# Performance work log

Hardware: AMD Instinct MI355X
Metric: run time of the kernel (lower is better)

Reference implementation:

```python
import jax, jax.numpy as jnp
import numpy as np
from jax import lax

N_QUBITS = 8
DIM = 256  # 2**8 amplitudes
NUM_BLOCKS = 16
DEPTH = 1
ALPHA = 0.5
BATCH = 512

# Z-sign tables: qubit 0 is the most-significant bit of the flattened state index
_bits = (np.arange(DIM)[:, None] >> (N_QUBITS - 1 - np.arange(N_QUBITS))) & 1  # (256, 8)
_SIGNS = jnp.asarray(1.0 - 2.0 * _bits, dtype=jnp.float32)  # (256, 8)
_pairs = [(i, j) for i in range(N_QUBITS) for j in range(i + 1, N_QUBITS)]
_PAIR_SIGNS = jnp.stack([_SIGNS[:, i] * _SIGNS[:, j] for (i, j) in _pairs], axis=1)  # (256, 28)


def _apply_ry(state, c, s, q):
    # state: (N, 256) real (RY and CNOT keep the state real); gate on qubit q
    dl, dr = 2 ** q, 2 ** (N_QUBITS - 1 - q)
    st = state.reshape(-1, dl, 2, dr)
    s0, s1 = st[:, :, 0, :], st[:, :, 1, :]
    c_, s_ = c[:, None, None], s[:, None, None]
    n0 = c_ * s0 - s_ * s1
    n1 = s_ * s0 + c_ * s1
    return jnp.stack([n0, n1], axis=2).reshape(-1, DIM)


def _apply_cnot_chain(state, i):
    # CNOT control=i, target=i+1 (adjacent qubits)
    dl, dr = 2 ** i, 2 ** (N_QUBITS - 2 - i)
    st = state.reshape(-1, dl, 2, 2, dr)
    c0 = st[:, :, 0]                  # control=0: unchanged
    c1 = st[:, :, 1][:, :, ::-1]      # control=1: flip target bit
    return jnp.stack([c0, c1], axis=2).reshape(-1, DIM)


def _quantum_map(theta):
    # theta: (N, 8) -> (N, 36) [Z_i expectations (8) then Z_i Z_j for i<j (28)]
    half = 0.5 * theta
    c, s = jnp.cos(half), jnp.sin(half)
    state = jnp.zeros((theta.shape[0], DIM), dtype=theta.dtype).at[:, 0].set(1.0)
    for q in range(N_QUBITS):
        state = _apply_ry(state, c[:, q], s[:, q], q)
    for _ in range(DEPTH):
        for i in range(N_QUBITS - 1):
            state = _apply_cnot_chain(state, i)
    p = state * state  # probabilities (state is real)
    single = p @ _SIGNS          # (N, 8)
    two_body = p @ _PAIR_SIGNS   # (N, 28)
    return jnp.concatenate([single, two_body], axis=1)


def _bn(x, g, b, m, v):
    # inference-mode BatchNorm2d, eps=1e-5
    inv = g / jnp.sqrt(v + 1e-5)
    return x * inv[None, :, None, None] + (b - m * inv)[None, :, None, None]


def _conv(x, w, b):
    y = lax.conv_general_dilated(x, w, (1, 1), 'SAME',
                                 dimension_numbers=('NCHW', 'OIHW', 'NCHW'))
    return y + b[None, :, None, None]


def _maxpool2(x):
    return lax.reduce_window(x, -jnp.inf, lax.max, (1, 1, 2, 2), (1, 1, 2, 2), 'VALID')


def setup_inputs() -> dict:
    key = jax.random.key(0)
    ks = jax.random.split(key, 8)
    f32 = jnp.float32
    return {
        'x': jax.random.normal(ks[0], (BATCH, 3, 64, 64), dtype=f32),
        'conv1_w': jax.random.normal(ks[1], (16, 3, 3, 3), dtype=f32) * 0.1,
        'conv1_b': jnp.zeros((16,), f32),
        'bn1_g': jnp.ones((16,), f32), 'bn1_b': jnp.zeros((16,), f32),
        'bn1_m': jnp.zeros((16,), f32), 'bn1_v': jnp.ones((16,), f32),
        'conv2_w': jax.random.normal(ks[2], (32, 16, 3, 3), dtype=f32) * 0.08,
        'conv2_b': jnp.zeros((32,), f32),
        'bn2_g': jnp.ones((32,), f32), 'bn2_b': jnp.zeros((32,), f32),
        'bn2_m': jnp.zeros((32,), f32), 'bn2_v': jnp.ones((32,), f32),
        'conv3_w': jax.random.normal(ks[3], (64, 32, 3, 3), dtype=f32) * 0.06,
        'conv3_b': jnp.zeros((64,), f32),
        'bn3_g': jnp.ones((64,), f32), 'bn3_b': jnp.zeros((64,), f32),
        'bn3_m': jnp.zeros((64,), f32), 'bn3_v': jnp.ones((64,), f32),
        'proj_w': jax.random.normal(ks[4], (NUM_BLOCKS, 256, N_QUBITS), dtype=f32) * 0.06,
        'proj_b': jnp.zeros((NUM_BLOCKS, N_QUBITS), f32),
        'cls_w': jax.random.normal(ks[5], (10, NUM_BLOCKS * 36), dtype=f32) * 0.04,
        'cls_b': jnp.zeros((10,), f32),
    }


def reference(x, conv1_w, conv1_b, bn1_g, bn1_b, bn1_m, bn1_v,
              conv2_w, conv2_b, bn2_g, bn2_b, bn2_m, bn2_v,
              conv3_w, conv3_b, bn3_g, bn3_b, bn3_m, bn3_v,
              proj_w, proj_b, cls_w, cls_b):
    h = _maxpool2(jax.nn.relu(_bn(_conv(x, conv1_w, conv1_b), bn1_g, bn1_b, bn1_m, bn1_v)))
    h = _maxpool2(jax.nn.relu(_bn(_conv(h, conv2_w, conv2_b), bn2_g, bn2_b, bn2_m, bn2_v)))
    h = _maxpool2(jax.nn.relu(_bn(_conv(h, conv3_w, conv3_b), bn3_g, bn3_b, bn3_m, bn3_v)))
    B = h.shape[0]
    feats = h.reshape(B, NUM_BLOCKS, 256)  # 16 chunks of 256
    z = jnp.einsum('bkc,kcd->bkd', feats, proj_w) + proj_b[None]  # (B, 16, 8)
    theta = ALPHA * jnp.tanh(z)
    q_out = _quantum_map(theta.reshape(B * NUM_BLOCKS, N_QUBITS))  # (B*16, 36)
    combined = q_out.reshape(B, NUM_BLOCKS * 36)
    return combined @ cls_w.T + cls_b
```

## Files before the change

kernel.cpp:

```cpp
#include <hip/hip_runtime.h>
#include <hip/hip_bf16.h>
#include <math.h>

typedef __attribute__((ext_vector_type(8))) short short8;
typedef __attribute__((ext_vector_type(4))) float f32x4;

__device__ __forceinline__ unsigned short f2bf(float f) {
    union { float f; unsigned u; } x; x.f = f;
    unsigned r = x.u + 0x7FFF + ((x.u >> 16) & 1);
    return (unsigned short)(r >> 16);
}

__device__ __forceinline__ short8 mk8(uint2 a, uint2 b) {
    union { uint2 u[2]; short8 s; } x;
    x.u[0] = a; x.u[1] = b;
    return x.s;
}

__global__ void k_prep(const float* __restrict__ w2, const float* __restrict__ w3,
    const float* g2, const float* be2, const float* m2, const float* v2, const float* cb2,
    const float* g3, const float* be3, const float* m3, const float* v3, const float* cb3,
    const float* __restrict__ w1,
    const float* g1, const float* be1, const float* m1, const float* v1, const float* cb1,
    const float* __restrict__ pjw,
    unsigned short* __restrict__ wp2, unsigned short* __restrict__ wp3,
    unsigned short* __restrict__ wp1,
    float* __restrict__ cst2, float* __restrict__ cst3, float* __restrict__ cst1,
    float* __restrict__ pjwt)
{
    int tid = blockIdx.x * 256 + threadIdx.x;
    if (tid < 5120) {
        int j = tid & 7, lane = (tid >> 3) & 63, o = (tid >> 9) & 1, s = tid >> 10;
        int kl = ((lane >> 4) << 3) + j;
        int tp = s * 2 + (kl >> 4);
        int ic = kl & 15;
        int oc = o * 16 + (lane & 15);
        float val = (tp < 9) ? w2[(oc * 16 + ic) * 9 + tp] : 0.f;
        wp2[tid] = f2bf(val);
    } else if (tid < 23552) {
        int idx = tid - 5120;
        int j = idx & 7, lane = (idx >> 3) & 63, o = (idx >> 9) & 3, tap = idx >> 11;
        int ic = ((lane >> 4) << 3) + j;
        int oc = o * 16 + (lane & 15);
        wp3[idx] = f2bf(w3[(oc * 32 + ic) * 9 + tap]);
    } else if (tid < 23648) {
        int c = tid - 23552;
        if (c < 32) {
            float inv = g2[c] * rsqrtf(v2[c] + 1e-5f);
            cst2[c] = inv;
            cst2[32 + c] = (cb2[c] - m2[c]) * inv + be2[c];
        } else {
            int c3 = c - 32;
            float inv = g3[c3] * rsqrtf(v3[c3] + 1e-5f);
            cst3[c3] = inv;
            cst3[64 + c3] = (cb3[c3] - m3[c3]) * inv + be3[c3];
        }
    } else if (tid < 24672) {
        int idx = tid - 23648;
        int j = idx & 7, lane = (idx >> 3) & 63, s = (idx >> 9) & 1;
        int k = ((lane >> 4) << 3) + j;
        int oc = lane & 15;
        float val = 0.f;
        if (s == 0) {
            int tap = k >> 2, ic = k & 3;
            if (ic < 3) val = w1[(oc * 3 + ic) * 9 + tap];
        } else {
            if (k < 3) val = w1[(oc * 3 + k) * 9 + 8];
        }
        wp1[idx] = f2bf(val);
    } else if (tid < 24688) {
        int c = tid - 24672;
        float inv = g1[c] * rsqrtf(v1[c] + 1e-5f);
        cst1[c] = inv;
        cst1[16 + c] = (cb1[c] - m1[c]) * inv + be1[c];
    } else if (tid < 57456) {
        int idx = tid - 24688;
        int k = idx >> 11, d = (idx >> 8) & 7, c = idx & 255;
        pjwt[idx] = pjw[k * 2048 + c * 8 + d];
    }
}

__global__ __launch_bounds__(512, 4) void k_fused(
    const float* __restrict__ x,
    const unsigned short* __restrict__ wp1, const float* __restrict__ cst1,
    const unsigned short* __restrict__ wp2, const float* __restrict__ cst2,
    const unsigned short* __restrict__ wp3, const float* __restrict__ cst3,
    const float* __restrict__ pjwt, const float* __restrict__ pjb,
    const float* __restrict__ cw, const float* __restrict__ cbias,
    float* __restrict__ out)
{
    __shared__ __align__(16) unsigned char smem[57728];
    unsigned short* xs   = (unsigned short*)smem;
    unsigned short* h2tA = (unsigned short*)smem;
    unsigned short* h2tB = (unsigned short*)(smem + 10368);
    unsigned short* h1A  = (unsigned short*)(smem + 20736);
    unsigned short* h1B  = (unsigned short*)(smem + 39232);
    float* feats = (float*)(smem + 20736);
    float* czs   = (float*)(smem + 20736 + 17408);
    float* partl = czs + 128;

    int b = blockIdx.x, t = threadIdx.x;
    int lane = t & 63, w = t >> 6, q = lane >> 4, xl = lane & 15;
    const float* img = x + (size_t)b * 12288;

    if (t < 264) {
        int arr = t & 1, idx = t >> 1;
        int y, xx;
        if (idx < 34)       { y = 0;        xx = idx; }
        else if (idx < 68)  { y = 33;       xx = idx - 34; }
        else if (idx < 100) { y = idx - 67; xx = 0; }
        else                { y = idx - 99; xx = 33; }
        uint4 z = {0u, 0u, 0u, 0u};
        *(uint4*)((arr ? h1B : h1A) + (y * 34 + xx) * 8) = z;
    }

    short8 A10 = *(const short8*)(wp1 + (lane << 3));
    short8 A11 = *(const short8*)(wp1 + ((64 + lane) << 3));
    int t0 = 2 * q, t1 = 2 * q + 1;
    int dy0 = t0 / 3 - 1, dx0 = t0 % 3 - 1;
    int dy1 = t1 / 3 - 1, dx1 = t1 % 3 - 1;
    float inv1[4], bs1[4];
    #pragma unroll
    for (int reg = 0; reg < 4; ++reg) {
        inv1[reg] = cst1[q * 4 + reg];
        bs1[reg]  = cst1[16 + q * 4 + reg];
    }
    unsigned* h1w = (unsigned*)(q < 2 ? h1A : h1B);
    #pragma unroll 1
    for (int h = 0; h < 2; ++h) {
        if (h) __syncthreads();
        int y0 = h * 32 - 1;
        #pragma unroll 1
        for (int i = 0; i < 5; ++i) {
            int idx = t + i * 512;
            if (idx < 2244) {
                int y = idx / 66, xx = idx - y * 66;
                int gy = y0 + y, gx = xx - 1;
                float v0 = 0.f, v1 = 0.f, v2 = 0.f;
                if ((unsigned)gy < 64u && (unsigned)gx < 64u) {
                    const float* pb = img + gy * 64 + gx;
                    v0 = pb[0]; v1 = pb[4096]; v2 = pb[8192];
                }
                uint2 pk;
                pk.x = (unsigned)f2bf(v0) | ((unsigned)f2bf(v1) << 16);
                pk.y = (unsigned)f2bf(v2);
                ((uint2*)xs)[idx] = pk;
            }
        }
        __syncthreads();
        #pragma unroll 1
        for (int xT = 0; xT < 4; ++xT) {
            int xb = xT * 16 + xl + 1;
            float pv[4], vo[4];
            #pragma unroll
            for (int r = 0; r < 4; ++r) {
                int ly = w * 4 + r + 1;
                const uint2* base = (const uint2*)xs;
                uint2 ua = base[(ly + dy0) * 66 + xb + dx0];
                uint2 ub = base[(ly + dy1) * 66 + xb + dx1];
                uint2 uc = base[(ly + 1) * 66 + xb + 1];
                f32x4 acc = (f32x4){0.f, 0.f, 0.f, 0.f};
                acc = __builtin_amdgcn_mfma_f32_16x16x32_bf16(A10, mk8(ua, ub), acc, 0, 0, 0);
                acc = __builtin_amdgcn_mfma_f32_16x16x32_bf16(A11, mk8(uc, uc), acc, 0, 0, 0);
                #pragma unroll
                for (int reg = 0; reg < 4; ++reg) {
                    float val = fmaxf(acc[reg] * inv1[reg] + bs1[reg], 0.f);
                    if (r & 1) {
                        float vm = fmaxf(val, pv[reg]);
                        vo[reg] = fmaxf(vm, __shfl_xor(vm, 1, 64));
                    } else {
                        pv[reg] = val;
                    }
                }
                if ((r & 1) && !(lane & 1)) {
                    int py = h * 16 + w * 2 + (r >> 1);
                    int px = xT * 8 + (xl >> 1);
                    int pos = (py + 1) * 34 + (px + 1);
                    unsigned u0 = (unsigned)f2bf(vo[0]) | ((unsigned)f2bf(vo[1]) << 16);
                    unsigned u1 = (unsigned)f2bf(vo[2]) | ((unsigned)f2bf(vo[3]) << 16);
                    unsigned* hp = h1w + pos * 4 + (q & 1) * 2;
                    hp[0] = u0; hp[1] = u1;
                }
            }
        }
    }
    __syncthreads();

    if (t < 264) {
        int idx = t >> 1, half = t & 1;
        int y, xx;
        if (idx < 18)      { y = 0;        xx = idx; }
        else if (idx < 36) { y = 17;       xx = idx - 18; }
        else if (idx < 52) { y = idx - 35; xx = 0; }
        else if (idx < 68) { y = idx - 51; xx = 17; }
        else { y = -1; xx = 0; }
        if (y >= 0) {
            uint4 z = {0u, 0u, 0u, 0u};
            int pos = y * 18 + xx;
            *(uint4*)((half ? h2tB : h2tA) + pos * 16) = z;
            *(uint4*)((half ? h2tB : h2tA) + pos * 16 + 8) = z;
        }
    }
    short8 A2[5][2];
    #pragma unroll
    for (int s = 0; s < 5; ++s)
        #pragma unroll
        for (int o = 0; o < 2; ++o)
            A2[s][o] = *(const short8*)(wp2 + (((s * 2 + o) * 64 + lane) << 3));
    int dyA[5], dxA[5];
    #pragma unroll
    for (int s = 0; s < 5; ++s) {
        int tp = s * 2 + (q >> 1); if (tp > 8) tp = 8;
        int d3 = tp / 3;
        dyA[s] = d3 - 1; dxA[s] = tp - d3 * 3 - 1;
    }
    {
        const unsigned short* h1r = (q & 1) ? h1B : h1A;
        f32x4 acc[4][2][2];
        #pragma unroll
        for (int r = 0; r < 4; ++r)
            #pragma unroll
            for (int xT = 0; xT < 2; ++xT)
                #pragma unroll
                for (int o = 0; o < 2; ++o)
                    acc[r][xT][o] = (f32x4){0.f, 0.f, 0.f, 0.f};
        #pragma unroll
        for (int r = 0; r < 4; ++r) {
            int ry = w * 4 + r;
            #pragma unroll
            for (int xT = 0; xT < 2; ++xT) {
                int gxb = xT * 16 + xl;
                #pragma unroll
                for (int s = 0; s < 5; ++s) {
                    int pos = (ry + dyA[s] + 1) * 34 + (gxb + dxA[s] + 1);
                    short8 B = *(const short8*)(h1r + pos * 8);
                    acc[r][xT][0] = __builtin_amdgcn_mfma_f32_16x16x32_bf16(A2[s][0], B, acc[r][xT][0], 0, 0, 0);
                    acc[r][xT][1] = __builtin_amdgcn_mfma_f32_16x16x32_bf16(A2[s][1], B, acc[r][xT][1], 0, 0, 0);
                }
            }
        }
        #pragma unroll
        for (int oT = 0; oT < 2; ++oT)
            #pragma unroll
            for (int rp = 0; rp < 2; ++rp)
                #pragma unroll
                for (int xT = 0; xT < 2; ++xT) {
                    float vo[4];
                    #pragma unroll
                    for (int reg = 0; reg < 4; ++reg) {
                        int oc = oT * 16 + q * 4 + reg;
                        float inv = cst2[oc], bs = cst2[32 + oc];
                        float v0 = fmaxf(acc[rp * 2][xT][oT][reg] * inv + bs, 0.f);
                        float v1 = fmaxf(acc[rp * 2 + 1][xT][oT][reg] * inv + bs, 0.f);
                        float vm = fmaxf(v0, v1);
                        vo[reg] = fmaxf(vm, __shfl_xor(vm, 1, 64));
                    }
                    if (!(lane & 1)) {
                        int py = w * 2 + rp;
                        int px = xT * 8 + (xl >> 1);
                        int pos = (py + 1) * 18 + (px + 1);
                        unsigned u0 = (unsigned)f2bf(vo[0]) | ((unsigned)f2bf(vo[1]) << 16);
                        unsigned u1 = (unsigned)f2bf(vo[2]) | ((unsigned)f2bf(vo[3]) << 16);
                        unsigned* hp = (unsigned*)(oT ? h2tB : h2tA) + pos * 8 + q * 2;
                        hp[0] = u0; hp[1] = u1;
                    }
                }
    }
    __syncthreads();

    {
        int op = w & 1, rg = w >> 1;
        const unsigned short* h2r = (q < 2) ? h2tA : h2tB;
        short8 A3[9][2];
        #pragma unroll
        for (int tap = 0; tap < 9; ++tap)
            #pragma unroll
            for (int tt = 0; tt < 2; ++tt)
                A3[tap][tt] = *(const short8*)(wp3 + (((tap * 4 + op * 2 + tt) * 64 + lane) << 3));
        f32x4 acc[4][2];
        #pragma unroll
        for (int r = 0; r < 4; ++r) {
            acc[r][0] = (f32x4){0.f, 0.f, 0.f, 0.f};
            acc[r][1] = (f32x4){0.f, 0.f, 0.f, 0.f};
        }
        #pragma unroll
        for (int r = 0; r < 4; ++r) {
            int ry = rg * 4 + r + 1;
            #pragma unroll
            for (int tap = 0; tap < 9; ++tap) {
                int pos = (ry + tap / 3 - 1) * 18 + xl + (tap % 3);
                short8 B = *(const short8*)(h2r + pos * 16 + (q & 1) * 8);
                acc[r][0] = __builtin_amdgcn_mfma_f32_16x16x32_bf16(A3[tap][0], B, acc[r][0], 0, 0, 0);
                acc[r][1] = __builtin_amdgcn_mfma_f32_16x16x32_bf16(A3[tap][1], B, acc[r][1], 0, 0, 0);
            }
        }
        #pragma unroll
        for (int tt = 0; tt < 2; ++tt)
            #pragma unroll
            for (int reg = 0; reg < 4; ++reg) {
                int oc = (op * 2 + tt) * 16 + q * 4 + reg;
                float inv = cst3[oc], bs = cst3[64 + oc];
                #pragma unroll
                for (int rp = 0; rp < 2; ++rp) {
                    float v0 = fmaxf(acc[rp * 2][tt][reg] * inv + bs, 0.f);
                    float v1 = fmaxf(acc[rp * 2 + 1][tt][reg] * inv + bs, 0.f);
                    float vm = fmaxf(v0, v1);
                    float vv = fmaxf(vm, __shfl_xor(vm, 1, 64));
                    if (!(lane & 1))
                        feats[oc * 68 + (rg * 2 + rp) * 8 + (xl >> 1)] = vv;
                }
            }
    }
    __syncthreads();

    if (t < 128) {
        int k = t >> 3, d = t & 7;
        const float4* wrow = (const float4*)(pjwt + (k * 8 + d) * 256);
        float zacc = 0.f;
        #pragma unroll 4
        for (int i = 0; i < 64; ++i) {
            int c4 = (i + k) & 63;
            float4 wv = wrow[c4];
            const float* fp = &feats[(k * 4 + (c4 >> 4)) * 68 + 4 * (c4 & 15)];
            float4 fv = *(const float4*)fp;
            zacc = fmaf(wv.x, fv.x, zacc);
            zacc = fmaf(wv.y, fv.y, zacc);
            zacc = fmaf(wv.z, fv.z, zacc);
            zacc = fmaf(wv.w, fv.w, zacc);
        }
        float z = zacc + pjb[k * 8 + d];
        czs[k * 8 + d] = cosf(0.5f * tanhf(z));
    }
    __syncthreads();
    if (t < 160) {
        int k = t / 10, c = t - (t / 10) * 10;
        float cz[8];
        #pragma unroll
        for (int i = 0; i < 8; ++i) cz[i] = czs[k * 8 + i];
        const float* cwp = cw + c * 576 + k * 36;
        float s = 0.f;
        float pp = 1.f;
        #pragma unroll
        for (int i = 0; i < 8; ++i) { pp *= cz[i]; s = fmaf(pp, cwp[i], s); }
        int cnt = 8;
        #pragma unroll
        for (int i = 0; i < 8; ++i) {
            float p2 = 1.f;
            #pragma unroll
            for (int j = i + 1; j < 8; ++j) { p2 *= cz[j]; s = fmaf(p2, cwp[cnt++], s); }
        }
        partl[k * 10 + c] = s;
    }
    __syncthreads();
    if (t < 10) {
        float s = cbias[t];
        #pragma unroll
        for (int k = 0; k < 16; ++k) s += partl[k * 10 + t];
        out[b * 10 + t] = s;
    }
}

extern "C" void kernel_launch(void* const* d_in, const int* in_sizes, int n_in,
                              void* d_out, int out_size, void* d_ws, size_t ws_size,
                              hipStream_t stream) {
    const float* x     = (const float*)d_in[0];
    const float* c1w   = (const float*)d_in[1];
    const float* c1b   = (const float*)d_in[2];
    const float* b1g   = (const float*)d_in[3];
    const float* b1b   = (const float*)d_in[4];
    const float* b1m   = (const float*)d_in[5];
    const float* b1v   = (const float*)d_in[6];
    const float* c2w   = (const float*)d_in[7];
    const float* c2b   = (const float*)d_in[8];
    const float* b2g   = (const float*)d_in[9];
    const float* b2b   = (const float*)d_in[10];
    const float* b2m   = (const float*)d_in[11];
    const float* b2v   = (const float*)d_in[12];
    const float* c3w   = (const float*)d_in[13];
    const float* c3b   = (const float*)d_in[14];
    const float* b3g   = (const float*)d_in[15];
    const float* b3b   = (const float*)d_in[16];
    const float* b3m   = (const float*)d_in[17];
    const float* b3v   = (const float*)d_in[18];
    const float* pjw   = (const float*)d_in[19];
    const float* pjb   = (const float*)d_in[20];
    const float* cw    = (const float*)d_in[21];
    const float* cbias = (const float*)d_in[22];
    float* outp = (float*)d_out;

    unsigned char* prep = (unsigned char*)d_ws;
    unsigned short* wp2 = (unsigned short*)prep;
    unsigned short* wp3 = (unsigned short*)(prep + 16384);
    unsigned short* wp1 = (unsigned short*)(prep + 16384 + 36864);
    float* cst2 = (float*)(prep + 16384 + 36864 + 2048);
    float* cst3 = cst2 + 64;
    float* cst1 = cst3 + 128;
    float* pjwt = (float*)(prep + 16384 + 36864 + 2048 + 1024);

    k_prep<<<225, 256, 0, stream>>>(c2w, c3w, b2g, b2b, b2m, b2v, c2b,
                                    b3g, b3b, b3m, b3v, c3b,
                                    c1w, b1g, b1b, b1m, b1v, c1b, pjw,
                                    wp2, wp3, wp1, cst2, cst3, cst1, pjwt);
    k_fused<<<512, 512, 0, stream>>>(x, wp1, cst1, wp2, cst2, wp3, cst3,
                                     pjwt, pjb, cw, cbias, outp);
}
```

Before: 138.8 us.

## Split conv inputs into even/odd column planes so pooling pairs share a lane

Stores the input tile and the conv1 output in separate even-column and odd-column shared-memory planes. Each lane can then compute both horizontal pooling partners (two phases) and take the max in registers instead of using cross-lane shuffles and half-idle stores. Conv2 reads the parity planes the same way, so its 2x2 pool also happens in registers and every lane writes. Float-to-bf16 packing now uses the paired conversion intrinsic. The trade-offs are more index arithmetic, doubled per-lane MFMA work per iteration, and possible changes in LDS bank-conflict patterns.

After: 136.9 us (median of 2 runs). About the same (-1.3%).

```diff
diff --git a/kernel.cpp b/kernel.cpp
--- a/kernel.cpp
+++ b/kernel.cpp
@@ -9,6 +9,12 @@
     union { float f; unsigned u; } x; x.f = f;
     unsigned r = x.u + 0x7FFF + ((x.u >> 16) & 1);
     return (unsigned short)(r >> 16);
+}
+
+__device__ __forceinline__ unsigned pk2bf(float a, float b) {
+    union { __hip_bfloat162 h; unsigned u; } x;
+    x.h = __float22bfloat162_rn(make_float2(a, b));
+    return x.u;
 }
 
 __device__ __forceinline__ short8 mk8(uint2 a, uint2 b) {
@@ -90,11 +96,11 @@
     float* __restrict__ out)
 {
     __shared__ __align__(16) unsigned char smem[57728];
-    unsigned short* xs   = (unsigned short*)smem;
+    uint2* xse = (uint2*)smem;
+    uint2* xso = xse + 34 * 33;
     unsigned short* h2tA = (unsigned short*)smem;
     unsigned short* h2tB = (unsigned short*)(smem + 10368);
-    unsigned short* h1A  = (unsigned short*)(smem + 20736);
-    unsigned short* h1B  = (unsigned short*)(smem + 39232);
+    unsigned short* h1s  = (unsigned short*)(smem + 20736);
     float* feats = (float*)(smem + 20736);
     float* czs   = (float*)(smem + 20736 + 17408);
     float* partl = czs + 128;
@@ -104,14 +110,13 @@
     const float* img = x + (size_t)b * 12288;
 
     if (t < 264) {
-        int arr = t & 1, idx = t >> 1;
-        int y, xx;
-        if (idx < 34)       { y = 0;        xx = idx; }
-        else if (idx < 68)  { y = 33;       xx = idx - 34; }
-        else if (idx < 100) { y = idx - 67; xx = 0; }
-        else                { y = idx - 99; xx = 33; }
+        int arr = t & 3, idx = t >> 2;
+        int row, slot;
+        if (idx < 17)      { row = 0;        slot = idx; }
+        else if (idx < 34) { row = 33;       slot = idx - 17; }
+        else               { row = idx - 33; slot = (arr & 1) ? 0 : 16; }
         uint4 z = {0u, 0u, 0u, 0u};
-        *(uint4*)((arr ? h1B : h1A) + (y * 34 + xx) * 8) = z;
+        *(uint4*)(h1s + arr * 4624 + (row * 17 + slot) * 8) = z;
     }
 
     short8 A10 = *(const short8*)(wp1 + (lane << 3));
@@ -125,66 +130,70 @@
         inv1[reg] = cst1[q * 4 + reg];
         bs1[reg]  = cst1[16 + q * 4 + reg];
     }
-    unsigned* h1w = (unsigned*)(q < 2 ? h1A : h1B);
     #pragma unroll 1
     for (int h = 0; h < 2; ++h) {
-        if (h) __syncthreads();
         int y0 = h * 32 - 1;
         #pragma unroll 1
         for (int i = 0; i < 5; ++i) {
             int idx = t + i * 512;
             if (idx < 2244) {
                 int y = idx / 66, xx = idx - y * 66;
-                int gy = y0 + y, gx = xx - 1;
+                int c = xx - 1;
+                int gy = y0 + y;
                 float v0 = 0.f, v1 = 0.f, v2 = 0.f;
-                if ((unsigned)gy < 64u && (unsigned)gx < 64u) {
-                    const float* pb = img + gy * 64 + gx;
+                if ((unsigned)gy < 64u && (unsigned)c < 64u) {
+                    const float* pb = img + gy * 64 + c;
                     v0 = pb[0]; v1 = pb[4096]; v2 = pb[8192];
                 }
                 uint2 pk;
-                pk.x = (unsigned)f2bf(v0) | ((unsigned)f2bf(v1) << 16);
-                pk.y = (unsigned)f2bf(v2);
-                ((uint2*)xs)[idx] = pk;
+                pk.x = pk2bf(v0, v1);
+                pk.y = pk2bf(v2, 0.f);
+                int par = c & 1, slot = (c + par) >> 1;
+                (par ? xso : xse)[y * 33 + slot] = pk;
             }
         }
         __syncthreads();
+        unsigned* h1wbase = (unsigned*)(h1s + (q >> 1) * 2 * 4624);
         #pragma unroll 1
-        for (int xT = 0; xT < 4; ++xT) {
-            int xb = xT * 16 + xl + 1;
-            float pv[4], vo[4];
+        for (int xTp = 0; xTp < 2; ++xTp) {
+            int X = xTp * 16 + xl;
+            float pv[4], vph[4];
             #pragma unroll
             for (int r = 0; r < 4; ++r) {
                 int ly = w * 4 + r + 1;
-                const uint2* base = (const uint2*)xs;
-                uint2 ua = base[(ly + dy0) * 66 + xb + dx0];
-                uint2 ub = base[(ly + dy1) * 66 + xb + dx1];
-                uint2 uc = base[(ly + 1) * 66 + xb + 1];
-                f32x4 acc = (f32x4){0.f, 0.f, 0.f, 0.f};
-                acc = __builtin_amdgcn_mfma_f32_16x16x32_bf16(A10, mk8(ua, ub), acc, 0, 0, 0);
-                acc = __builtin_amdgcn_mfma_f32_16x16x32_bf16(A11, mk8(uc, uc), acc, 0, 0, 0);
                 #pragma unroll
-                for (int reg = 0; reg < 4; ++reg) {
-                    float val = fmaxf(acc[reg] * inv1[reg] + bs1[reg], 0.f);
-                    if (r & 1) {
-                        float vm = fmaxf(val, pv[reg]);
-                        vo[reg] = fmaxf(vm, __shfl_xor(vm, 1, 64));
-                    } else {
-                        pv[reg] = val;
+                for (int ph = 0; ph < 2; ++ph) {
+                    int e0 = ph + dx0, e1 = ph + dx1, e2 = ph + 1;
+                    const uint2* p0 = (e0 & 1) ? xso : xse;
+                    const uint2* p1 = (e1 & 1) ? xso : xse;
+                    const uint2* p2 = (e2 & 1) ? xso : xse;
+                    uint2 ua = p0[(ly + dy0) * 33 + X + ((e0 + 1) >> 1)];
+                    uint2 ub = p1[(ly + dy1) * 33 + X + ((e1 + 1) >> 1)];
+                    uint2 uc = p2[(ly + 1) * 33 + X + ((e2 + 1) >> 1)];
+                    f32x4 acc = (f32x4){0.f, 0.f, 0.f, 0.f};
+                    acc = __builtin_amdgcn_mfma_f32_16x16x32_bf16(A10, mk8(ua, ub), acc, 0, 0, 0);
+                    acc = __builtin_amdgcn_mfma_f32_16x16x32_bf16(A11, mk8(uc, uc), acc, 0, 0, 0);
+                    #pragma unroll
+                    for (int reg = 0; reg < 4; ++reg) {
+                        float val = fmaxf(acc[reg] * inv1[reg] + bs1[reg], 0.f);
+                        vph[reg] = ph ? fmaxf(vph[reg], val) : val;
                     }
                 }
-                if ((r & 1) && !(lane & 1)) {
+                if (r & 1) {
                     int py = h * 16 + w * 2 + (r >> 1);
-                    int px = xT * 8 + (xl >> 1);
-                    int pos = (py + 1) * 34 + (px + 1);
-                    unsigned u0 = (unsigned)f2bf(vo[0]) | ((unsigned)f2bf(vo[1]) << 16);
-                    unsigned u1 = (unsigned)f2bf(vo[2]) | ((unsigned)f2bf(vo[3]) << 16);
-                    unsigned* hp = h1w + pos * 4 + (q & 1) * 2;
-                    hp[0] = u0; hp[1] = u1;
-                }
-            }
-        }
-    }
-    __syncthreads();
+                    int par = X & 1, slot = (X >> 1) + par;
+                    unsigned* hp = h1wbase + par * 2312
+                                   + ((py + 1) * 17 + slot) * 4 + (q & 1) * 2;
+                    hp[0] = pk2bf(fmaxf(vph[0], pv[0]), fmaxf(vph[1], pv[1]));
+                    hp[1] = pk2bf(fmaxf(vph[2], pv[2]), fmaxf(vph[3], pv[3]));
+                } else {
+                    #pragma unroll
+                    for (int reg = 0; reg < 4; ++reg) pv[reg] = vph[reg];
+                }
+            }
+        }
+        __syncthreads();
+    }
 
     if (t < 264) {
         int idx = t >> 1, half = t & 1;
@@ -201,70 +210,67 @@
             *(uint4*)((half ? h2tB : h2tA) + pos * 16 + 8) = z;
         }
     }
-    short8 A2[5][2];
-    #pragma unroll
-    for (int s = 0; s < 5; ++s)
-        #pragma unroll
-        for (int o = 0; o < 2; ++o)
-            A2[s][o] = *(const short8*)(wp2 + (((s * 2 + o) * 64 + lane) << 3));
-    int dyA[5], dxA[5];
-    #pragma unroll
-    for (int s = 0; s < 5; ++s) {
-        int tp = s * 2 + (q >> 1); if (tp > 8) tp = 8;
-        int d3 = tp / 3;
-        dyA[s] = d3 - 1; dxA[s] = tp - d3 * 3 - 1;
-    }
+
     {
-        const unsigned short* h1r = (q & 1) ? h1B : h1A;
+        short8 A2[5][2];
+        #pragma unroll
+        for (int s = 0; s < 5; ++s)
+            #pragma unroll
+            for (int o = 0; o < 2; ++o)
+                A2[s][o] = *(const short8*)(wp2 + (((s * 2 + o) * 64 + lane) << 3));
+        int dyA[5], dxA[5];
+        #pragma unroll
+        for (int s = 0; s < 5; ++s) {
+            int tp = s * 2 + (q >> 1); if (tp > 8) tp = 8;
+            int d3 = tp / 3;
+            dyA[s] = d3 - 1; dxA[s] = tp - d3 * 3 - 1;
+        }
+        const unsigned short* hb = h1s + (q & 1) * 2 * 4624;
         f32x4 acc[4][2][2];
         #pragma unroll
         for (int r = 0; r < 4; ++r)
             #pragma unroll
-            for (int xT = 0; xT < 2; ++xT)
+            for (int ph = 0; ph < 2; ++ph)
                 #pragma unroll
                 for (int o = 0; o < 2; ++o)
-                    acc[r][xT][o] = (f32x4){0.f, 0.f, 0.f, 0.f};
+                    acc[r][ph][o] = (f32x4){0.f, 0.f, 0.f, 0.f};
         #pragma unroll
         for (int r = 0; r < 4; ++r) {
             int ry = w * 4 + r;
             #pragma unroll
-            for (int xT = 0; xT < 2; ++xT) {
-                int gxb = xT * 16 + xl;
+            for (int ph = 0; ph < 2; ++ph) {
                 #pragma unroll
                 for (int s = 0; s < 5; ++s) {
-                    int pos = (ry + dyA[s] + 1) * 34 + (gxb + dxA[s] + 1);
-                    short8 B = *(const short8*)(h1r + pos * 8);
-                    acc[r][xT][0] = __builtin_amdgcn_mfma_f32_16x16x32_bf16(A2[s][0], B, acc[r][xT][0], 0, 0, 0);
-                    acc[r][xT][1] = __builtin_amdgcn_mfma_f32_16x16x32_bf16(A2[s][1], B, acc[r][xT][1], 0, 0, 0);
+                    int e = ph + dxA[s];
+                    int row = ry + dyA[s] + 1;
+                    int slot = xl + ((e + 1) >> 1);
+                    const unsigned short* src = hb + (e & 1) * 4624;
+                    short8 B = *(const short8*)(src + (row * 17 + slot) * 8);
+                    acc[r][ph][0] = __builtin_amdgcn_mfma_f32_16x16x32_bf16(A2[s][0], B, acc[r][ph][0], 0, 0, 0);
+                    acc[r][ph][1] = __builtin_amdgcn_mfma_f32_16x16x32_bf16(A2[s][1], B, acc[r][ph][1], 0, 0, 0);
                 }
             }
         }
         #pragma unroll
         for (int oT = 0; oT < 2; ++oT)
             #pragma unroll
-            for (int rp = 0; rp < 2; ++rp)
+            for (int rp = 0; rp < 2; ++rp) {
+                float vo[4];
                 #pragma unroll
-                for (int xT = 0; xT < 2; ++xT) {
-                    float vo[4];
-                    #pragma unroll
-                    for (int reg = 0; reg < 4; ++reg) {
-                        int oc = oT * 16 + q * 4 + reg;
-                        float inv = cst2[oc], bs = cst2[32 + oc];
-                        float v0 = fmaxf(acc[rp * 2][xT][oT][reg] * inv + bs, 0.f);
-                        float v1 = fmaxf(acc[rp * 2 + 1][xT][oT][reg] * inv + bs, 0.f);
-                        float vm = fmaxf(v0, v1);
-                        vo[reg] = fmaxf(vm, __shfl_xor(vm, 1, 64));
-                    }
-                    if (!(lane & 1)) {
-                        int py = w * 2 + rp;
-                        int px = xT * 8 + (xl >> 1);
-                        int pos = (py + 1) * 18 + (px + 1);
-                        unsigned u0 = (unsigned)f2bf(vo[0]) | ((unsigned)f2bf(vo[1]) << 16);
-                        unsigned u1 = (unsigned)f2bf(vo[2]) | ((unsigned)f2bf(vo[3]) << 16);
-                        unsigned* hp = (unsigned*)(oT ? h2tB : h2tA) + pos * 8 + q * 2;
-                        hp[0] = u0; hp[1] = u1;
-                    }
-                }
+                for (int reg = 0; reg < 4; ++reg) {
+                    int oc = oT * 16 + q * 4 + reg;
+                    float iv = cst2[oc], bv = cst2[32 + oc];
+                    float v00 = fmaxf(acc[rp * 2][0][oT][reg] * iv + bv, 0.f);
+                    float v01 = fmaxf(acc[rp * 2][1][oT][reg] * iv + bv, 0.f);
+                    float v10 = fmaxf(acc[rp * 2 + 1][0][oT][reg] * iv + bv, 0.f);
+                    float v11 = fmaxf(acc[rp * 2 + 1][1][oT][reg] * iv + bv, 0.f);
+                    vo[reg] = fmaxf(fmaxf(v00, v01), fmaxf(v10, v11));
+                }
+                int pos = (w * 2 + rp + 1) * 18 + (xl + 1);
+                unsigned* hp = (unsigned*)(oT ? h2tB : h2tA) + pos * 8 + q * 2;
+                hp[0] = pk2bf(vo[0], vo[1]);
+                hp[1] = pk2bf(vo[2], vo[3]);
+            }
     }
     __syncthreads();
 
@@ -299,11 +305,11 @@
             #pragma unroll
             for (int reg = 0; reg < 4; ++reg) {
                 int oc = (op * 2 + tt) * 16 + q * 4 + reg;
-                float inv = cst3[oc], bs = cst3[64 + oc];
+                float iv = cst3[oc], bv = cst3[64 + oc];
                 #pragma unroll
                 for (int rp = 0; rp < 2; ++rp) {
-                    float v0 = fmaxf(acc[rp * 2][tt][reg] * inv + bs, 0.f);
-                    float v1 = fmaxf(acc[rp * 2 + 1][tt][reg] * inv + bs, 0.f);
+                    float v0 = fmaxf(acc[rp * 2][tt][reg] * iv + bv, 0.f);
+                    float v1 = fmaxf(acc[rp * 2 + 1][tt][reg] * iv + bv, 0.f);
                     float vm = fmaxf(v0, v1);
                     float vv = fmaxf(vm, __shfl_xor(vm, 1, 64));
                     if (!(lane & 1))
@@ -315,7 +321,7 @@
 
     if (t < 128) {
         int k = t >> 3, d = t & 7;
-        const float4* wrow = (const float4*)(pjwt + (k * 8 + d) * 256);
+        const float4* wrow = (const float4*)(pjwt + ((k * 8 + d) << 8));
         float zacc = 0.f;
         #pragma unroll 4
         for (int i = 0; i < 64; ++i) {
```
